# Optimization experiments

Hardware: AMD Instinct MI355X
Metric: run time of the kernel (lower is better)

Reference implementation:

```python
import jax, jax.numpy as jnp
from jax import lax
import numpy as np

SIZE = 512           # self.size in the torch module
N_PHOS = 256         # number of phosphenes
MAX_RADIUS = 15.0    # radii in [3,15] -> sigma = r/3 <= 5 -> half = ceil(2*sigma) <= 10
H = 10               # static max half kernel width (torchvision kernel_size = 2*ceil(2*sigma)+1)
THRESH = 0.05


def setup_inputs() -> dict:
    key = jax.random.key(0)
    k1, k2, k3 = jax.random.split(key, 3)
    # grid columns: [x, y, radius], already in 512-pixel space (imgsize=512 -> scale 1)
    xy = jax.random.uniform(k1, (N_PHOS, 2), minval=20.0, maxval=SIZE - 20.0, dtype=jnp.float32)
    radii = jax.random.uniform(k2, (N_PHOS,), minval=3.0, maxval=MAX_RADIUS, dtype=jnp.float32)
    grid = jnp.concatenate([xy, radii[:, None]], axis=1)  # (n, 3)
    phoscoding = jax.random.uniform(k3, (N_PHOS,), dtype=jnp.float32)  # brightness in [0,1)
    return {"phoscoding": phoscoding, "grid": grid}


def _one_phosphene(brightness, x, y, r):
    # Circle mask. In the torch code (meshgrid 'ij', 1-based coords):
    #   mask[i, j] = (j+1 - x)^2 + (i+1 - y)^2 <= r^2
    c = jnp.arange(1, SIZE + 1, dtype=jnp.float32)
    mask = ((c[None, :] - x) ** 2 + (c[:, None] - y) ** 2) <= r ** 2
    phos = mask.astype(jnp.float32) * brightness  # (512, 512)

    # torchvision GaussianBlur kernel: linspace(-k/2..k/2) == integer offsets here,
    # pdf = exp(-0.5*(t/sigma)^2), normalized. Emulate the data-dependent kernel_size
    # by zeroing taps beyond half = ceil(2*sigma) inside a static width 2H+1 kernel.
    sigma = r / 3.0
    half = jnp.ceil(2.0 * sigma)
    pos = jnp.arange(-H, H + 1, dtype=jnp.float32)
    w = jnp.exp(-0.5 * (pos / sigma) ** 2) * (jnp.abs(pos) <= half)
    w = w / jnp.sum(w)

    # Reflect padding (torchvision pads kernel_size//2 with 'reflect'; padding H with the
    # extra taps zeroed is mathematically identical since reflect values depend only on
    # distance from the edge).
    pad = jnp.pad(phos, H, mode='reflect')[None, None]            # (1,1,512+2H,512+2H)
    out = lax.conv(pad, w.reshape(1, 1, 2 * H + 1, 1), (1, 1), 'VALID')
    out = lax.conv(out, w.reshape(1, 1, 1, 2 * H + 1), (1, 1), 'VALID')[0, 0]  # (512,512)

    return jnp.where(out < THRESH, 0.0, out)


def reference(phoscoding, grid):
    x, y, r = grid[:, 0], grid[:, 1], grid[:, 2]
    per_phos = jax.vmap(_one_phosphene)(phoscoding, x, y, r)  # (n, 512, 512)
    img = jnp.sum(per_phos, axis=0)
    img = jnp.minimum(img, 1.0)           # img[img > 1] = 1
    m = jnp.max(img)
    img = jnp.where(m > 0, img / m, img)  # normalize unless all-zero
    return img[None, None]                # (1, 1, 512, 512)
```

## Files before the change

kernel.cpp:

```cpp
#include <hip/hip_runtime.h>


#define SIZE   512
#define NPIX   (SIZE * SIZE)
#define H      10
#define KW     21
#define THRESH 0.05f

__global__ __launch_bounds__(256) void zero_k(float* __restrict__ img,
                                              unsigned* __restrict__ mx)
{
  int i = blockIdx.x * 256 + threadIdx.x;
  ((float4*)img)[i] = make_float4(0.f, 0.f, 0.f, 0.f);
  if (i == 0) *mx = 0u;
}

__global__ __launch_bounds__(256) void phos_accum(
    const float* __restrict__ pc, const float* __restrict__ grid,
    float* __restrict__ img)
{
  __shared__ float vert[51 * 32];

  const int p = blockIdx.x;
  const float x = grid[3 * p + 0];
  const float y = grid[3 * p + 1];
  const float r = grid[3 * p + 2];
  const float b = pc[p];

  const float sigma = r / 3.0f;
  const float halfw = ceilf(2.0f * sigma);
  float w[KW];
  float s = 0.0f;
#pragma unroll
  for (int t = 0; t < KW; ++t) {
    float pos = (float)(t - H);
    float wt = (fabsf(pos) <= halfw)
                   ? expf(-0.5f * (pos / sigma) * (pos / sigma))
                   : 0.0f;
    w[t] = wt;
    s += wt;
  }
#pragma unroll
  for (int t = 0; t < KW; ++t) w[t] /= s;

  const float cx = x - 1.0f;
  const float cy = y - 1.0f;
  int icmin = max((int)ceilf(cx - r), 0);
  int icmax = min((int)floorf(cx + r), SIZE - 1);
  int irmin = max((int)ceilf(cy - r), 0);
  int irmax = min((int)floorf(cy + r), SIZE - 1);
  const int ox0 = max(0, icmin - H), ox1 = min(SIZE - 1, icmax + H);
  const int oy0 = max(0, irmin - H), oy1 = min(SIZE - 1, irmax + H);
  const int ncol = icmax - icmin + 1;
  const int nrow = oy1 - oy0 + 1;
  const float r2 = r * r;

  for (int idx = threadIdx.x; idx < nrow * ncol; idx += blockDim.x) {
    int cj = idx / ncol;
    int ci = idx - cj * ncol;
    int c  = icmin + ci;
    float dx  = (float)c - cx;
    float dx2 = dx * dx;
    int j = oy0 + cj;
    float acc = 0.0f;
#pragma unroll
    for (int t = 0; t < KW; ++t) {
      int jj = j + (t - H);
      jj = (jj < 0) ? -jj : ((jj > SIZE - 1) ? 2 * (SIZE - 1) - jj : jj);
      float dy = (float)jj - cy;
      acc += (dx2 + dy * dy <= r2) ? w[t] : 0.0f;
    }
    vert[cj * 32 + ci] = acc;
  }
  __syncthreads();

  const int nox = ox1 - ox0 + 1;
  for (int idx = threadIdx.x; idx < nrow * nox; idx += blockDim.x) {
    int cj = idx / nox;
    int ci = idx - cj * nox;
    int i = ox0 + ci;
    int j = oy0 + cj;
    float acc = 0.0f;
#pragma unroll
    for (int t = 0; t < KW; ++t) {
      int ii = i + (t - H);
      ii = (ii < 0) ? -ii : ((ii > SIZE - 1) ? 2 * (SIZE - 1) - ii : ii);
      int cc = ii - icmin;
      if ((unsigned)cc < (unsigned)ncol) acc += w[t] * vert[cj * 32 + cc];
    }
    float val = acc * b;
    if (val >= THRESH) atomicAdd(&img[j * SIZE + i], val);
  }
}

__global__ __launch_bounds__(256) void max_k(const float* __restrict__ img,
                                             unsigned* __restrict__ mx)
{
  __shared__ float smax[4];
  const float4* im4 = (const float4*)img;
  float m = 0.0f;
  for (int i = blockIdx.x * 256 + threadIdx.x; i < NPIX / 4;
       i += gridDim.x * 256) {
    float4 v = im4[i];
    m = fmaxf(m, fmaxf(fmaxf(v.x, v.y), fmaxf(v.z, v.w)));
  }
#pragma unroll
  for (int off = 32; off > 0; off >>= 1)
    m = fmaxf(m, __shfl_down(m, off, 64));
  if ((threadIdx.x & 63) == 0) smax[threadIdx.x >> 6] = m;
  __syncthreads();
  if (threadIdx.x == 0) {
    m = fmaxf(fmaxf(smax[0], smax[1]), fmaxf(smax[2], smax[3]));
    atomicMax(mx, __float_as_uint(m));
  }
}

__global__ __launch_bounds__(256) void norm_clip_k(
    float* __restrict__ img, const unsigned* __restrict__ mx)
{
  int i = blockIdx.x * 256 + threadIdx.x;
  float m = fminf(__uint_as_float(*mx), 1.0f);
  float4 v = ((float4*)img)[i];
  v.x = fminf(v.x, 1.0f);
  v.y = fminf(v.y, 1.0f);
  v.z = fminf(v.z, 1.0f);
  v.w = fminf(v.w, 1.0f);
  if (m > 0.0f) {
    v.x /= m; v.y /= m; v.z /= m; v.w /= m;
  }
  ((float4*)img)[i] = v;
}

extern "C" void kernel_launch(void* const* d_in, const int* in_sizes, int n_in,
                              void* d_out, int out_size, void* d_ws, size_t ws_size,
                              hipStream_t stream)
{
  const float* pc   = (const float*)d_in[0];
  const float* grid = (const float*)d_in[1];
  float* img   = (float*)d_out;
  unsigned* mx = (unsigned*)d_ws;

  zero_k<<<NPIX / (256 * 4), 256, 0, stream>>>(img, mx);
  phos_accum<<<256, 256, 0, stream>>>(pc, grid, img);
  max_k<<<64, 256, 0, stream>>>(img, mx);
  norm_clip_k<<<NPIX / (256 * 4), 256, 0, stream>>>(img, mx);
}
```

Before: 82.66 us.

## Precompute reflect-extended vertical pass to remove branches from horizontal convolution

The vertical pass now writes a row buffer already extended by the horizontal halo, with reflect indexing resolved at that stage. This lets the horizontal pass run a branch-free 21-tap dot product over contiguous shared memory. The max reduction is unrolled into four fixed loads per thread, and the normalize kernel multiplies by a reciprocal instead of dividing. The extended buffer computes more vertical entries (many of them zero) and uses more shared memory; the reciprocal multiply can differ slightly in rounding from division.

```diff
diff --git a/kernel.cpp b/kernel.cpp
--- a/kernel.cpp
+++ b/kernel.cpp
@@ -19,9 +19,10 @@
     const float* __restrict__ pc, const float* __restrict__ grid,
     float* __restrict__ img)
 {
-  __shared__ float vert[51 * 32];
+  __shared__ float ext[51 * 72];
 
   const int p = blockIdx.x;
+  const int t = threadIdx.x;
   const float x = grid[3 * p + 0];
   const float y = grid[3 * p + 1];
   const float r = grid[3 * p + 2];
@@ -32,64 +33,63 @@
   float w[KW];
   float s = 0.0f;
 #pragma unroll
-  for (int t = 0; t < KW; ++t) {
-    float pos = (float)(t - H);
+  for (int k = 0; k < KW; ++k) {
+    float pos = (float)(k - H);
     float wt = (fabsf(pos) <= halfw)
                    ? expf(-0.5f * (pos / sigma) * (pos / sigma))
                    : 0.0f;
-    w[t] = wt;
+    w[k] = wt;
     s += wt;
   }
 #pragma unroll
-  for (int t = 0; t < KW; ++t) w[t] /= s;
+  for (int k = 0; k < KW; ++k) w[k] /= s;
 
-  const float cx = x - 1.0f;
-  const float cy = y - 1.0f;
-  int icmin = max((int)ceilf(cx - r), 0);
-  int icmax = min((int)floorf(cx + r), SIZE - 1);
-  int irmin = max((int)ceilf(cy - r), 0);
-  int irmax = min((int)floorf(cy + r), SIZE - 1);
+  const float cx = x - 1.0f, cy = y - 1.0f;
+  const int icmin = max((int)ceilf(cx - r), 0);
+  const int icmax = min((int)floorf(cx + r), SIZE - 1);
+  const int irmin = max((int)ceilf(cy - r), 0);
+  const int irmax = min((int)floorf(cy + r), SIZE - 1);
   const int ox0 = max(0, icmin - H), ox1 = min(SIZE - 1, icmax + H);
   const int oy0 = max(0, irmin - H), oy1 = min(SIZE - 1, irmax + H);
   const int ncol = icmax - icmin + 1;
   const int nrow = oy1 - oy0 + 1;
+  const int nox  = ox1 - ox0 + 1;
+  const int next = nox + 2 * H;
   const float r2 = r * r;
 
-  for (int idx = threadIdx.x; idx < nrow * ncol; idx += blockDim.x) {
-    int cj = idx / ncol;
-    int ci = idx - cj * ncol;
-    int c  = icmin + ci;
-    float dx  = (float)c - cx;
-    float dx2 = dx * dx;
-    int j = oy0 + cj;
-    float acc = 0.0f;
+  for (int idx = t; idx < nrow * next; idx += 256) {
+    int cj = idx / next;
+    int e  = idx - cj * next;
+    int ii = ox0 - H + e;
+    ii = (ii < 0) ? -ii : ((ii > SIZE - 1) ? 2 * (SIZE - 1) - ii : ii);
+    int cc = ii - icmin;
+    float a = 0.0f;
+    if ((unsigned)cc < (unsigned)ncol) {
+      float dx  = (float)ii - cx;
+      float dx2 = dx * dx;
+      int j = oy0 + cj;
 #pragma unroll
-    for (int t = 0; t < KW; ++t) {
-      int jj = j + (t - H);
-      jj = (jj < 0) ? -jj : ((jj > SIZE - 1) ? 2 * (SIZE - 1) - jj : jj);
-      float dy = (float)jj - cy;
-      acc += (dx2 + dy * dy <= r2) ? w[t] : 0.0f;
+      for (int k = 0; k < KW; ++k) {
+        int jj = j + (k - H);
+        jj = (jj < 0) ? -jj : ((jj > SIZE - 1) ? 2 * (SIZE - 1) - jj : jj);
+        float dy = (float)jj - cy;
+        a += (dx2 + dy * dy <= r2) ? w[k] : 0.0f;
+      }
     }
-    vert[cj * 32 + ci] = acc;
+    ext[cj * 72 + e] = a;
   }
   __syncthreads();
 
-  const int nox = ox1 - ox0 + 1;
-  for (int idx = threadIdx.x; idx < nrow * nox; idx += blockDim.x) {
+  for (int idx = t; idx < nrow * nox; idx += 256) {
     int cj = idx / nox;
     int ci = idx - cj * nox;
-    int i = ox0 + ci;
-    int j = oy0 + cj;
-    float acc = 0.0f;
+    const float* erow = &ext[cj * 72 + ci];
+    float a = 0.0f;
 #pragma unroll
-    for (int t = 0; t < KW; ++t) {
-      int ii = i + (t - H);
-      ii = (ii < 0) ? -ii : ((ii > SIZE - 1) ? 2 * (SIZE - 1) - ii : ii);
-      int cc = ii - icmin;
-      if ((unsigned)cc < (unsigned)ncol) acc += w[t] * vert[cj * 32 + cc];
-    }
-    float val = acc * b;
-    if (val >= THRESH) atomicAdd(&img[j * SIZE + i], val);
+    for (int k = 0; k < KW; ++k) a += w[k] * erow[k];
+    float val = a * b;
+    if (val >= THRESH)
+      atomicAdd(&img[(oy0 + cj) * SIZE + ox0 + ci], val);
   }
 }
 
@@ -98,12 +98,16 @@
 {
   __shared__ float smax[4];
   const float4* im4 = (const float4*)img;
-  float m = 0.0f;
-  for (int i = blockIdx.x * 256 + threadIdx.x; i < NPIX / 4;
-       i += gridDim.x * 256) {
-    float4 v = im4[i];
-    m = fmaxf(m, fmaxf(fmaxf(v.x, v.y), fmaxf(v.z, v.w)));
-  }
+  const int i0 = blockIdx.x * 256 + threadIdx.x;
+  const int stride = 64 * 256;
+  float4 v0 = im4[i0];
+  float4 v1 = im4[i0 + stride];
+  float4 v2 = im4[i0 + 2 * stride];
+  float4 v3 = im4[i0 + 3 * stride];
+  float m = fmaxf(fmaxf(fmaxf(v0.x, v0.y), fmaxf(v0.z, v0.w)),
+                  fmaxf(fmaxf(v1.x, v1.y), fmaxf(v1.z, v1.w)));
+  m = fmaxf(m, fmaxf(fmaxf(fmaxf(v2.x, v2.y), fmaxf(v2.z, v2.w)),
+                     fmaxf(fmaxf(v3.x, v3.y), fmaxf(v3.z, v3.w))));
 #pragma unroll
   for (int off = 32; off > 0; off >>= 1)
     m = fmaxf(m, __shfl_down(m, off, 64));
@@ -120,14 +124,12 @@
 {
   int i = blockIdx.x * 256 + threadIdx.x;
   float m = fminf(__uint_as_float(*mx), 1.0f);
+  float inv = (m > 0.0f) ? 1.0f / m : 1.0f;
   float4 v = ((float4*)img)[i];
-  v.x = fminf(v.x, 1.0f);
-  v.y = fminf(v.y, 1.0f);
-  v.z = fminf(v.z, 1.0f);
-  v.w = fminf(v.w, 1.0f);
-  if (m > 0.0f) {
-    v.x /= m; v.y /= m; v.z /= m; v.w /= m;
-  }
+  v.x = fminf(v.x, 1.0f) * inv;
+  v.y = fminf(v.y, 1.0f) * inv;
+  v.z = fminf(v.z, 1.0f) * inv;
+  v.w = fminf(v.w, 1.0f) * inv;
   ((float4*)img)[i] = v;
 }
 
@@ -136,12 +138,12 @@
                               hipStream_t stream)
 {
   const float* pc   = (const float*)d_in[0];
-  const float* grid = (const float*)d_in[1];
+  const float* grd  = (const float*)d_in[1];
   float* img   = (float*)d_out;
   unsigned* mx = (unsigned*)d_ws;
 
   zero_k<<<NPIX / (256 * 4), 256, 0, stream>>>(img, mx);
-  phos_accum<<<256, 256, 0, stream>>>(pc, grid, img);
+  phos_accum<<<256, 256, 0, stream>>>(pc, grd, img);
   max_k<<<64, 256, 0, stream>>>(img, mx);
   norm_clip_k<<<NPIX / (256 * 4), 256, 0, stream>>>(img, mx);
 }
```

Measured after the change: 74.80 us. -9.5%, faster.
